# Kernel tuning notes

Measured on AMD Instinct MI355X. Metric: run time of the kernel, lower is better.

Reference implementation:

```python
import jax, jax.numpy as jnp
import numpy as np

N = 262144          # num nodes
D = 512             # embedding dim
H = 8               # attention heads
C = 4096            # num components (segments)


def setup_inputs() -> dict:
    key = jax.random.key(0)
    k1, k2, k3 = jax.random.split(key, 3)
    feats = jax.random.normal(k1, (N, D), dtype=jnp.float32)
    component_id = jnp.sort(jax.random.randint(k2, (N,), 0, C, dtype=jnp.int64))
    attn_w = jax.random.normal(k3, (D, H), dtype=jnp.float32) / np.sqrt(D)
    attn_b = jnp.zeros((H,), dtype=jnp.float32)
    return {
        "feats": feats,
        "component_id": component_id,
        "attn_w": attn_w,
        "attn_b": attn_b,
        "num_components": C,
    }


def _segment_attention_pool(feats, seg, attn_w, attn_b, num_segments):
    """Multi-head attention readout: softmax over nodes within each segment,
    weighted sum of head-split features. feats: [N, D], seg: [N] int."""
    n, d = feats.shape
    h = attn_w.shape[1]
    dh = d // h
    # Per-node, per-head attention logits: [N, H]
    scores = feats @ attn_w + attn_b
    # Numerically stable segment softmax
    seg_max = jax.ops.segment_max(scores, seg, num_segments=num_segments)  # [C, H]
    exp = jnp.exp(scores - seg_max[seg])                                   # [N, H]
    denom = jax.ops.segment_sum(exp, seg, num_segments=num_segments)       # [C, H]
    weights = exp / denom[seg]                                             # [N, H]
    # Weighted segment-sum of head-split features -> [C, H, Dh] -> [C, D]
    weighted = weights[:, :, None] * feats.reshape(n, h, dh)
    pooled = jax.ops.segment_sum(weighted, seg, num_segments=num_segments)
    return pooled.reshape(num_segments, d), weights


def reference(feats, component_id, attn_w, attn_b, num_components):
    pooled, weights = _segment_attention_pool(
        feats, component_id, attn_w, attn_b, num_components
    )
    comp_ids = jnp.arange(num_components, dtype=jnp.int64)
    return pooled, comp_ids, weights
```

## Files before the change

kernel.cpp:

```cpp
#include <hip/hip_runtime.h>
#include <math.h>

#define DIM 512
#define NH 8
#define BLOCK 256
#define NWAVE 4

__device__ __forceinline__ float sel4(float a0, float a1, float a2, float a3, int k) {
  float r01 = (k & 1) ? a1 : a0;
  float r23 = (k & 1) ? a3 : a2;
  return (k & 2) ? r23 : r01;
}

__device__ __forceinline__ int lower_bound(const int* __restrict__ a, int n, int key) {
  int lo = 0, hi = n;
  while (lo < hi) {
    int mid = (lo + hi) >> 1;
    if (a[mid] < key) lo = mid + 1; else hi = mid;
  }
  return lo;
}

__global__ __launch_bounds__(BLOCK) void seg_attn_kernel(
    const float* __restrict__ feats,
    const int* __restrict__ seg,
    const float* __restrict__ attn_w,
    const float* __restrict__ attn_b,
    float* __restrict__ out,
    int N, int C, int idMode)
{
  const int c   = blockIdx.x;
  const int tid = threadIdx.x;
  const int w   = tid >> 6;
  const int t   = tid & 63;
  const int h1  = t >> 4;
  const int h2  = 4 + h1;

  float* pooled = out;
  float* compf  = out + (size_t)C * DIM;
  float* wbuf   = compf + (idMode ? 2 * (size_t)C : (size_t)C);

  if (tid == 0) {
    if (idMode) ((long long*)compf)[c] = (long long)c;
    else        compf[c] = (float)c;
  }

  const int start = lower_bound(seg, N, c);
  const int end   = lower_bound(seg, N, c + 1);

  float4 wA[4], wB[4], wC[4], wD[4];
#pragma unroll
  for (int e = 0; e < 4; ++e) {
    const float4* p0 = (const float4*)(attn_w + (size_t)(4 * t + e) * NH);
    wA[e] = p0[0];
    wB[e] = p0[1];
    const float4* p1 = (const float4*)(attn_w + (size_t)(256 + 4 * t + e) * NH);
    wC[e] = p1[0];
    wD[e] = p1[1];
  }
  float bias[NH];
#pragma unroll
  for (int h = 0; h < NH; ++h) bias[h] = attn_b[h];

  const float NEG = -3.0e38f;
  float m_[NH], l_[NH];
#pragma unroll
  for (int h = 0; h < NH; ++h) { m_[h] = NEG; l_[h] = 0.f; }
  float4 acc0 = make_float4(0.f, 0.f, 0.f, 0.f);
  float4 acc1 = make_float4(0.f, 0.f, 0.f, 0.f);

  for (int i = start + w; i < end; i += NWAVE) {
    const float4* fp = (const float4*)(feats + (size_t)i * DIM);
    float4 f0 = fp[t];
    float4 f1 = fp[64 + t];

    float s[NH];
#pragma unroll
    for (int h = 0; h < NH; ++h) s[h] = bias[h];
    {
      const float f0e[4] = {f0.x, f0.y, f0.z, f0.w};
      const float f1e[4] = {f1.x, f1.y, f1.z, f1.w};
#pragma unroll
      for (int e = 0; e < 4; ++e) {
        s[0] = fmaf(f0e[e], wA[e].x, s[0]);
        s[1] = fmaf(f0e[e], wA[e].y, s[1]);
        s[2] = fmaf(f0e[e], wA[e].z, s[2]);
        s[3] = fmaf(f0e[e], wA[e].w, s[3]);
        s[4] = fmaf(f0e[e], wB[e].x, s[4]);
        s[5] = fmaf(f0e[e], wB[e].y, s[5]);
        s[6] = fmaf(f0e[e], wB[e].z, s[6]);
        s[7] = fmaf(f0e[e], wB[e].w, s[7]);
        s[0] = fmaf(f1e[e], wC[e].x, s[0]);
        s[1] = fmaf(f1e[e], wC[e].y, s[1]);
        s[2] = fmaf(f1e[e], wC[e].z, s[2]);
        s[3] = fmaf(f1e[e], wC[e].w, s[3]);
        s[4] = fmaf(f1e[e], wD[e].x, s[4]);
        s[5] = fmaf(f1e[e], wD[e].y, s[5]);
        s[6] = fmaf(f1e[e], wD[e].z, s[6]);
        s[7] = fmaf(f1e[e], wD[e].w, s[7]);
      }
    }
#pragma unroll
    for (int off = 1; off < 64; off <<= 1) {
#pragma unroll
      for (int h = 0; h < NH; ++h) s[h] += __shfl_xor(s[h], off, 64);
    }

    if (t == 0) {
      float4* sp = (float4*)(wbuf + (size_t)i * NH);
      sp[0] = make_float4(s[0], s[1], s[2], s[3]);
      sp[1] = make_float4(s[4], s[5], s[6], s[7]);
    }

    float al[NH], p[NH];
#pragma unroll
    for (int h = 0; h < NH; ++h) {
      float mn = fmaxf(m_[h], s[h]);
      al[h] = __expf(m_[h] - mn);
      p[h]  = __expf(s[h] - mn);
      l_[h] = l_[h] * al[h] + p[h];
      m_[h] = mn;
    }
    float a1 = sel4(al[0], al[1], al[2], al[3], h1);
    float p1 = sel4(p[0],  p[1],  p[2],  p[3],  h1);
    float a2 = sel4(al[4], al[5], al[6], al[7], h1);
    float p2 = sel4(p[4],  p[5],  p[6],  p[7],  h1);
    acc0.x = fmaf(p1, f0.x, acc0.x * a1);
    acc0.y = fmaf(p1, f0.y, acc0.y * a1);
    acc0.z = fmaf(p1, f0.z, acc0.z * a1);
    acc0.w = fmaf(p1, f0.w, acc0.w * a1);
    acc1.x = fmaf(p2, f1.x, acc1.x * a2);
    acc1.y = fmaf(p2, f1.y, acc1.y * a2);
    acc1.z = fmaf(p2, f1.z, acc1.z * a2);
    acc1.w = fmaf(p2, f1.w, acc1.w * a2);
  }

  __shared__ float mlw[NWAVE][2 * NH];
  __shared__ float mf[NH], rl[NH];
  __shared__ float pool[NWAVE][DIM];

  if (t == 0) {
#pragma unroll
    for (int h = 0; h < NH; ++h) { mlw[w][h] = m_[h]; mlw[w][NH + h] = l_[h]; }
  }
  __syncthreads();
  if (tid < NH) {
    float mm = NEG;
#pragma unroll
    for (int q = 0; q < NWAVE; ++q) mm = fmaxf(mm, mlw[q][tid]);
    float ll = 0.f;
#pragma unroll
    for (int q = 0; q < NWAVE; ++q) ll += mlw[q][NH + tid] * __expf(mlw[q][tid] - mm);
    mf[tid] = mm;
    rl[tid] = (ll > 0.f) ? (1.f / ll) : 0.f;
  }
  __syncthreads();

  float mw1 = sel4(m_[0], m_[1], m_[2], m_[3], h1);
  float mw2 = sel4(m_[4], m_[5], m_[6], m_[7], h1);
  float sc1 = __expf(mw1 - mf[h1]);
  float sc2 = __expf(mw2 - mf[h2]);
  float* pw = &pool[w][4 * t];
  pw[0]   = acc0.x * sc1;  pw[1]   = acc0.y * sc1;
  pw[2]   = acc0.z * sc1;  pw[3]   = acc0.w * sc1;
  pw[256] = acc1.x * sc2;  pw[257] = acc1.y * sc2;
  pw[258] = acc1.z * sc2;  pw[259] = acc1.w * sc2;
  __syncthreads();

#pragma unroll
  for (int r = 0; r < 2; ++r) {
    int d = tid + r * 256;
    float v = pool[0][d] + pool[1][d] + pool[2][d] + pool[3][d];
    v *= rl[d >> 6];
    pooled[(size_t)c * DIM + d] = v;
  }

  for (int idx = start * NH + tid; idx < end * NH; idx += BLOCK) {
    int h = idx & 7;
    wbuf[idx] = __expf(wbuf[idx] - mf[h]) * rl[h];
  }
}

extern "C" void kernel_launch(void* const* d_in, const int* in_sizes, int n_in,
                              void* d_out, int out_size, void* d_ws, size_t ws_size,
                              hipStream_t stream) {
  const float* feats  = (const float*)d_in[0];
  const int*   seg    = (const int*)d_in[1];
  const float* attn_w = (const float*)d_in[2];
  const float* attn_b = (const float*)d_in[3];

  const int N  = in_sizes[1];
  const int Hh = in_sizes[3];
  const int Dd = in_sizes[2] / Hh;
  long long rem = (long long)out_size - (long long)N * Hh;

  int C, idMode;
  if (rem % (Dd + 1) == 0) { C = (int)(rem / (Dd + 1)); idMode = 0; }
  else                     { C = (int)(rem / (Dd + 2)); idMode = 1; }

  seg_attn_kernel<<<C, BLOCK, 0, stream>>>(feats, seg, attn_w, attn_b,
                                           (float*)d_out, N, C, idMode);
}
```

Before: 766.7 us.

## Process two rows per wave with head-per-lane-group layout and precomputed segment offsets

Each wave now handles two nodes per iteration. Each lane owns 8 contiguous features, which match a single head's slice, so the online softmax keeps one scalar max and sum per lane instead of eight. The logit reduction becomes an 8-lane butterfly followed by a transpose shuffle instead of a 64-lane reduction. A separate pass computes segment offsets into the workspace so the main kernel no longer binary-searches, and launch bounds request two blocks per CU. This adds an extra kernel launch and more registers per thread.

```diff
diff --git a/kernel.cpp b/kernel.cpp
--- a/kernel.cpp
+++ b/kernel.cpp
@@ -5,11 +5,28 @@
 #define NH 8
 #define BLOCK 256
 #define NWAVE 4
-
-__device__ __forceinline__ float sel4(float a0, float a1, float a2, float a3, int k) {
-  float r01 = (k & 1) ? a1 : a0;
-  float r23 = (k & 1) ? a3 : a2;
-  return (k & 2) ? r23 : r01;
+#define NEGF -3.0e38f
+
+__global__ void seg_offsets_kernel(const int* __restrict__ seg,
+                                   int* __restrict__ off, int N, int C) {
+  int i = blockIdx.x * blockDim.x + threadIdx.x;
+  if (i >= N) return;
+  int s = seg[i];
+  int snext = (i + 1 < N) ? seg[i + 1] : C;
+  for (int c = s + 1; c <= snext; ++c) off[c] = i + 1;
+  if (i == 0) {
+    for (int c = 0; c <= s; ++c) off[c] = 0;
+  }
+}
+
+__device__ __forceinline__ float sel8(const float* v, int k) {
+  float a = (k & 1) ? v[1] : v[0];
+  float b = (k & 1) ? v[3] : v[2];
+  float c = (k & 1) ? v[5] : v[4];
+  float d = (k & 1) ? v[7] : v[6];
+  float e = (k & 2) ? b : a;
+  float f = (k & 2) ? d : c;
+  return (k & 4) ? f : e;
 }
 
 __device__ __forceinline__ int lower_bound(const int* __restrict__ a, int n, int key) {
@@ -21,11 +38,12 @@
   return lo;
 }
 
-__global__ __launch_bounds__(BLOCK) void seg_attn_kernel(
+__global__ __launch_bounds__(BLOCK, 2) void seg_attn_kernel(
     const float* __restrict__ feats,
     const int* __restrict__ seg,
     const float* __restrict__ attn_w,
     const float* __restrict__ attn_b,
+    const int* __restrict__ off,
     float* __restrict__ out,
     int N, int C, int idMode)
 {
@@ -33,8 +51,8 @@
   const int tid = threadIdx.x;
   const int w   = tid >> 6;
   const int t   = tid & 63;
-  const int h1  = t >> 4;
-  const int h2  = 4 + h1;
+  const int g   = t >> 3;
+  const int j   = t & 7;
 
   float* pooled = out;
   float* compf  = out + (size_t)C * DIM;
@@ -45,107 +63,102 @@
     else        compf[c] = (float)c;
   }
 
-  const int start = lower_bound(seg, N, c);
-  const int end   = lower_bound(seg, N, c + 1);
-
-  float4 wA[4], wB[4], wC[4], wD[4];
-#pragma unroll
-  for (int e = 0; e < 4; ++e) {
-    const float4* p0 = (const float4*)(attn_w + (size_t)(4 * t + e) * NH);
-    wA[e] = p0[0];
-    wB[e] = p0[1];
-    const float4* p1 = (const float4*)(attn_w + (size_t)(256 + 4 * t + e) * NH);
-    wC[e] = p1[0];
-    wD[e] = p1[1];
-  }
-  float bias[NH];
-#pragma unroll
-  for (int h = 0; h < NH; ++h) bias[h] = attn_b[h];
-
-  const float NEG = -3.0e38f;
-  float m_[NH], l_[NH];
-#pragma unroll
-  for (int h = 0; h < NH; ++h) { m_[h] = NEG; l_[h] = 0.f; }
-  float4 acc0 = make_float4(0.f, 0.f, 0.f, 0.f);
-  float4 acc1 = make_float4(0.f, 0.f, 0.f, 0.f);
-
-  for (int i = start + w; i < end; i += NWAVE) {
-    const float4* fp = (const float4*)(feats + (size_t)i * DIM);
-    float4 f0 = fp[t];
-    float4 f1 = fp[64 + t];
-
-    float s[NH];
-#pragma unroll
-    for (int h = 0; h < NH; ++h) s[h] = bias[h];
-    {
-      const float f0e[4] = {f0.x, f0.y, f0.z, f0.w};
-      const float f1e[4] = {f1.x, f1.y, f1.z, f1.w};
-#pragma unroll
-      for (int e = 0; e < 4; ++e) {
-        s[0] = fmaf(f0e[e], wA[e].x, s[0]);
-        s[1] = fmaf(f0e[e], wA[e].y, s[1]);
-        s[2] = fmaf(f0e[e], wA[e].z, s[2]);
-        s[3] = fmaf(f0e[e], wA[e].w, s[3]);
-        s[4] = fmaf(f0e[e], wB[e].x, s[4]);
-        s[5] = fmaf(f0e[e], wB[e].y, s[5]);
-        s[6] = fmaf(f0e[e], wB[e].z, s[6]);
-        s[7] = fmaf(f0e[e], wB[e].w, s[7]);
-        s[0] = fmaf(f1e[e], wC[e].x, s[0]);
-        s[1] = fmaf(f1e[e], wC[e].y, s[1]);
-        s[2] = fmaf(f1e[e], wC[e].z, s[2]);
-        s[3] = fmaf(f1e[e], wC[e].w, s[3]);
-        s[4] = fmaf(f1e[e], wD[e].x, s[4]);
-        s[5] = fmaf(f1e[e], wD[e].y, s[5]);
-        s[6] = fmaf(f1e[e], wD[e].z, s[6]);
-        s[7] = fmaf(f1e[e], wD[e].w, s[7]);
+  int start, end;
+  if (off) { start = off[c]; end = off[c + 1]; }
+  else     { start = lower_bound(seg, N, c); end = lower_bound(seg, N, c + 1); }
+
+  float4 w0[8], w1[8];
+#pragma unroll
+  for (int e = 0; e < 8; ++e) {
+    const float4* p = (const float4*)(attn_w + (size_t)(8 * t + e) * NH);
+    w0[e] = p[0];
+    w1[e] = p[1];
+  }
+  const float bias_g = attn_b[g];
+
+  float m_ = NEGF, l_ = 0.f;
+  float acc[8];
+#pragma unroll
+  for (int e = 0; e < 8; ++e) acc[e] = 0.f;
+
+  for (int i0 = start + 2 * w; i0 < end; i0 += 2 * NWAVE) {
+    const int i1 = i0 + 1;
+    const bool v1 = (i1 < end);
+    const float4* r0 = (const float4*)(feats + (size_t)i0 * DIM);
+    const float4* r1 = (const float4*)(feats + (size_t)(v1 ? i1 : i0) * DIM);
+    float4 a0 = r0[2 * t], a1 = r0[2 * t + 1];
+    float4 b0 = r1[2 * t], b1 = r1[2 * t + 1];
+
+    float f1v[8] = {a0.x, a0.y, a0.z, a0.w, a1.x, a1.y, a1.z, a1.w};
+    float f2v[8] = {b0.x, b0.y, b0.z, b0.w, b1.x, b1.y, b1.z, b1.w};
+
+    float s1[NH], s2[NH];
+#pragma unroll
+    for (int h = 0; h < NH; ++h) { s1[h] = 0.f; s2[h] = 0.f; }
+#pragma unroll
+    for (int e = 0; e < 8; ++e) {
+      s1[0] = fmaf(f1v[e], w0[e].x, s1[0]);
+      s1[1] = fmaf(f1v[e], w0[e].y, s1[1]);
+      s1[2] = fmaf(f1v[e], w0[e].z, s1[2]);
+      s1[3] = fmaf(f1v[e], w0[e].w, s1[3]);
+      s1[4] = fmaf(f1v[e], w1[e].x, s1[4]);
+      s1[5] = fmaf(f1v[e], w1[e].y, s1[5]);
+      s1[6] = fmaf(f1v[e], w1[e].z, s1[6]);
+      s1[7] = fmaf(f1v[e], w1[e].w, s1[7]);
+      s2[0] = fmaf(f2v[e], w0[e].x, s2[0]);
+      s2[1] = fmaf(f2v[e], w0[e].y, s2[1]);
+      s2[2] = fmaf(f2v[e], w0[e].z, s2[2]);
+      s2[3] = fmaf(f2v[e], w0[e].w, s2[3]);
+      s2[4] = fmaf(f2v[e], w1[e].x, s2[4]);
+      s2[5] = fmaf(f2v[e], w1[e].y, s2[5]);
+      s2[6] = fmaf(f2v[e], w1[e].z, s2[6]);
+      s2[7] = fmaf(f2v[e], w1[e].w, s2[7]);
+    }
+#pragma unroll
+    for (int o = 1; o < 8; o <<= 1) {
+#pragma unroll
+      for (int h = 0; h < NH; ++h) {
+        s1[h] += __shfl_xor(s1[h], o, 64);
+        s2[h] += __shfl_xor(s2[h], o, 64);
       }
     }
-#pragma unroll
-    for (int off = 1; off < 64; off <<= 1) {
-#pragma unroll
-      for (int h = 0; h < NH; ++h) s[h] += __shfl_xor(s[h], off, 64);
-    }
-
-    if (t == 0) {
-      float4* sp = (float4*)(wbuf + (size_t)i * NH);
-      sp[0] = make_float4(s[0], s[1], s[2], s[3]);
-      sp[1] = make_float4(s[4], s[5], s[6], s[7]);
-    }
-
-    float al[NH], p[NH];
-#pragma unroll
-    for (int h = 0; h < NH; ++h) {
-      float mn = fmaxf(m_[h], s[h]);
-      al[h] = __expf(m_[h] - mn);
-      p[h]  = __expf(s[h] - mn);
-      l_[h] = l_[h] * al[h] + p[h];
-      m_[h] = mn;
-    }
-    float a1 = sel4(al[0], al[1], al[2], al[3], h1);
-    float p1 = sel4(p[0],  p[1],  p[2],  p[3],  h1);
-    float a2 = sel4(al[4], al[5], al[6], al[7], h1);
-    float p2 = sel4(p[4],  p[5],  p[6],  p[7],  h1);
-    acc0.x = fmaf(p1, f0.x, acc0.x * a1);
-    acc0.y = fmaf(p1, f0.y, acc0.y * a1);
-    acc0.z = fmaf(p1, f0.z, acc0.z * a1);
-    acc0.w = fmaf(p1, f0.w, acc0.w * a1);
-    acc1.x = fmaf(p2, f1.x, acc1.x * a2);
-    acc1.y = fmaf(p2, f1.y, acc1.y * a2);
-    acc1.z = fmaf(p2, f1.z, acc1.z * a2);
-    acc1.w = fmaf(p2, f1.w, acc1.w * a2);
+    float y1 = sel8(s1, j);
+    float y2 = sel8(s2, j);
+    const int src = (j << 3) | g;
+    y1 = __shfl(y1, src, 64);
+    y2 = __shfl(y2, src, 64);
+#pragma unroll
+    for (int o = 1; o < 8; o <<= 1) {
+      y1 += __shfl_xor(y1, o, 64);
+      y2 += __shfl_xor(y2, o, 64);
+    }
+    y1 += bias_g;
+    y2 = v1 ? (y2 + bias_g) : NEGF;
+
+    if (j == 0) {
+      wbuf[(size_t)i0 * NH + g] = y1;
+      if (v1) wbuf[(size_t)i1 * NH + g] = y2;
+    }
+
+    float mn = fmaxf(m_, fmaxf(y1, y2));
+    float al = __expf(m_ - mn);
+    float p1 = __expf(y1 - mn);
+    float p2 = __expf(y2 - mn);
+    l_ = l_ * al + p1 + p2;
+    m_ = mn;
+#pragma unroll
+    for (int e = 0; e < 8; ++e)
+      acc[e] = fmaf(p2, f2v[e], fmaf(p1, f1v[e], acc[e] * al));
   }
 
   __shared__ float mlw[NWAVE][2 * NH];
   __shared__ float mf[NH], rl[NH];
   __shared__ float pool[NWAVE][DIM];
 
-  if (t == 0) {
-#pragma unroll
-    for (int h = 0; h < NH; ++h) { mlw[w][h] = m_[h]; mlw[w][NH + h] = l_[h]; }
-  }
+  if (j == 0) { mlw[w][g] = m_; mlw[w][NH + g] = l_; }
   __syncthreads();
   if (tid < NH) {
-    float mm = NEG;
+    float mm = NEGF;
 #pragma unroll
     for (int q = 0; q < NWAVE; ++q) mm = fmaxf(mm, mlw[q][tid]);
     float ll = 0.f;
@@ -156,15 +169,12 @@
   }
   __syncthreads();
 
-  float mw1 = sel4(m_[0], m_[1], m_[2], m_[3], h1);
-  float mw2 = sel4(m_[4], m_[5], m_[6], m_[7], h1);
-  float sc1 = __expf(mw1 - mf[h1]);
-  float sc2 = __expf(mw2 - mf[h2]);
-  float* pw = &pool[w][4 * t];
-  pw[0]   = acc0.x * sc1;  pw[1]   = acc0.y * sc1;
-  pw[2]   = acc0.z * sc1;  pw[3]   = acc0.w * sc1;
-  pw[256] = acc1.x * sc2;  pw[257] = acc1.y * sc2;
-  pw[258] = acc1.z * sc2;  pw[259] = acc1.w * sc2;
+  const float sc = __expf(m_ - mf[g]);
+  {
+    float4* pw = (float4*)&pool[w][8 * t];
+    pw[0] = make_float4(acc[0] * sc, acc[1] * sc, acc[2] * sc, acc[3] * sc);
+    pw[1] = make_float4(acc[4] * sc, acc[5] * sc, acc[6] * sc, acc[7] * sc);
+  }
   __syncthreads();
 
 #pragma unroll
@@ -198,6 +208,11 @@
   if (rem % (Dd + 1) == 0) { C = (int)(rem / (Dd + 1)); idMode = 0; }
   else                     { C = (int)(rem / (Dd + 2)); idMode = 1; }
 
-  seg_attn_kernel<<<C, BLOCK, 0, stream>>>(feats, seg, attn_w, attn_b,
+  int* off = nullptr;
+  if (ws_size >= (size_t)(C + 1) * sizeof(int)) {
+    off = (int*)d_ws;
+    seg_offsets_kernel<<<(N + 255) / 256, 256, 0, stream>>>(seg, off, N, C);
+  }
+  seg_attn_kernel<<<C, BLOCK, 0, stream>>>(feats, seg, attn_w, attn_b, off,
                                            (float*)d_out, N, C, idMode);
 }
```

After: 750.7 us. 2.1% less time.
